# Performance work log

Hardware: AMD Instinct MI355X
Metric: run time of the kernel (lower is better)

Reference implementation:

```python
import jax, jax.numpy as jnp
import numpy as np

TEMP = 0.1
EPS = 1e-08

def _l2norm(x):
    # F.normalize semantics: x / max(||x||, 1e-12)
    n = jnp.linalg.norm(x, axis=-1, keepdims=True)
    return x / jnp.maximum(n, 1e-12)

def setup_inputs() -> dict:
    key = jax.random.key(0)
    k0, k1, k2, k3, k4 = jax.random.split(key, 5)
    B, Ph, Pw, D, O = 32, 32, 32, 512, 128
    P = Ph * Pw
    patch_features = jax.random.normal(k0, (B, Ph, Pw, D), jnp.float32)
    obj_features = jax.random.normal(k1, (B, O, D), jnp.float32)
    # e1i: each patch positively matched to one object (one-hot rows)
    idx = jax.random.randint(k2, (B, P), 0, O)
    e1i = jax.nn.one_hot(idx, O, dtype=jnp.float32)
    # e1j / e2j: sparse binary negative masks
    e1j = (jax.random.uniform(k3, (B, P, P)) < 0.1).astype(jnp.float32)
    e2j = (jax.random.uniform(k4, (B, P, O)) < 0.1).astype(jnp.float32)
    return {"patch_features": patch_features, "obj_features": obj_features,
            "e1i": e1i, "e1j": e1j, "e2j": e2j}

def reference(patch_features, obj_features, e1i, e1j, e2j):
    B, D = patch_features.shape[0], patch_features.shape[-1]
    pf = patch_features.reshape(B, -1, D)          # [B, P, D]
    pn = _l2norm(pf)
    on = _l2norm(obj_features)                     # [B, O, D]
    po_sim = jnp.einsum('bpd,bod->bpo', pn, on)    # patch-object cosine sim
    po_exp = jnp.exp(po_sim / TEMP)
    pp_exp = jnp.exp(jnp.einsum('bpd,bqd->bpq', pn, pn) / TEMP)
    delta_E1i_E2i = jnp.sum(e1i * po_exp, axis=-1)     # [B, P]
    sum_E1i_E1j = jnp.sum(e1j * pp_exp, axis=-1)
    sum_E1i_E2j = jnp.sum(e2j * po_exp, axis=-1)
    ratio = delta_E1i_E2i / (delta_E1i_E2i + sum_E1i_E1j + sum_E1i_E2j + EPS)
    loss_all = -jnp.log(ratio + EPS)                   # [B, P]
    valid = (jnp.sum(e1i, axis=-1) > 0).astype(loss_all.dtype)  # [B, P]
    n_valid = jnp.sum(valid)
    loss = jnp.sum(loss_all * valid) / n_valid
    matched = jnp.argmax(po_sim, axis=-1)              # [B, P]
    labels = jnp.take_along_axis(e1i, matched[..., None], axis=-1)[..., 0]
    matched_success_ratio = jnp.sum(labels * valid) / n_valid
    return loss, matched_success_ratio
```

## Files before the change

### kernel.cpp

```cpp
#include <hip/hip_runtime.h>
#include <hip/hip_bf16.h>

constexpr int BB = 32;
constexpr int P  = 1024;
constexpr int O  = 128;
constexpr int D  = 512;
constexpr float EPS = 1e-8f;
constexpr float SCL = 14.426950408889634f;

typedef __attribute__((ext_vector_type(8))) short short8;
typedef __attribute__((ext_vector_type(16))) float f32x16;

__device__ __forceinline__ unsigned short f2bf(float f) {
  __hip_bfloat16 h = __float2bfloat16(f);
  unsigned short u;
  __builtin_memcpy(&u, &h, sizeof(u));
  return u;
}

__device__ __forceinline__ void gld_lds16(const void* g, void* l) {
  __builtin_amdgcn_global_load_lds(
      (const __attribute__((address_space(1))) void*)g,
      (__attribute__((address_space(3))) void*)l, 16, 0, 0);
}

constexpr int FB = (BB * P + BB * O) / 4;
constexpr int JB = (BB * P) / 4;
__global__ __launch_bounds__(256) void prep2_kernel(
    const float* __restrict__ pf, const float* __restrict__ of,
    const float* __restrict__ e1i, const float* __restrict__ e1j,
    const float* __restrict__ e2j,
    __hip_bfloat16* __restrict__ pn, __hip_bfloat16* __restrict__ on,
    unsigned long long* __restrict__ bm1j, unsigned long long* __restrict__ bm2j,
    int* __restrict__ posr) {
  const int lane = threadIdx.x & 63;
  const int wid4 = threadIdx.x >> 6;
  const int bid  = blockIdx.x;

  if (bid < FB) {
    int row = bid * 4 + wid4;
    const float* src;
    __hip_bfloat16* dst;
    if (row < BB * P) {
      src = pf + (size_t)row * D;
      dst = pn + (size_t)row * D;
    } else {
      int r = row - BB * P;
      if (r >= BB * O) return;
      src = of + (size_t)r * D;
      dst = on + (size_t)r * D;
    }
    float4 v0 = *(const float4*)(src + lane * 8);
    float4 v1 = *(const float4*)(src + lane * 8 + 4);
    float ss = v0.x * v0.x + v0.y * v0.y + v0.z * v0.z + v0.w * v0.w +
               v1.x * v1.x + v1.y * v1.y + v1.z * v1.z + v1.w * v1.w;
    #pragma unroll
    for (int s = 1; s < 64; s <<= 1) ss += __shfl_xor(ss, s);
    float sc = 1.0f / fmaxf(sqrtf(ss), 1e-12f);
    short8 w;
    w[0] = (short)f2bf(v0.x * sc); w[1] = (short)f2bf(v0.y * sc);
    w[2] = (short)f2bf(v0.z * sc); w[3] = (short)f2bf(v0.w * sc);
    w[4] = (short)f2bf(v1.x * sc); w[5] = (short)f2bf(v1.y * sc);
    w[6] = (short)f2bf(v1.z * sc); w[7] = (short)f2bf(v1.w * sc);
    *reinterpret_cast<short8*>(dst + lane * 8) = w;
  } else if (bid < FB + JB) {
    const int row = (bid - FB) * 4 + wid4;
    const float* src = e1j + (size_t)row * P;
    #pragma unroll
    for (int it = 0; it < 16; ++it) {
      unsigned long long b = __ballot(src[it * 64 + lane] > 0.5f);
      if (lane == 0) bm1j[(size_t)row * 16 + it] = b;
    }
  } else {
    const int row = (bid - FB - JB) * 4 + wid4;
    unsigned long long b0 = __ballot(e1i[(size_t)row * O + lane] > 0.5f);
    unsigned long long b1 = __ballot(e1i[(size_t)row * O + 64 + lane] > 0.5f);
    unsigned long long d0 = __ballot(e2j[(size_t)row * O + lane] > 0.5f);
    unsigned long long d1 = __ballot(e2j[(size_t)row * O + 64 + lane] > 0.5f);
    if (lane == 0) {
      posr[row] = b0 ? (__ffsll(b0) - 1) : (b1 ? 63 + __ffsll(b1) : -1);
      bm2j[(size_t)row * 2]     = d0;
      bm2j[(size_t)row * 2 + 1] = d1;
    }
  }
}

__global__ __launch_bounds__(256, 3) void icl_main10(
    const __hip_bfloat16* __restrict__ pn, const __hip_bfloat16* __restrict__ on,
    const unsigned long long* __restrict__ bm1j,
    const unsigned long long* __restrict__ bm2j,
    const int* __restrict__ posr,
    float* __restrict__ d_row, float* __restrict__ s1_row,
    float* __restrict__ s2_row, unsigned long long* __restrict__ pk_row) {

  __shared__ __hip_bfloat16 As[128 * 64];
  __shared__ __hip_bfloat16 Bs[128 * 64];

  const int tid  = threadIdx.x;
  const int l    = tid & 63;
  const int wid  = tid >> 6;
  const int wr   = wid >> 1;
  const int wc   = wid & 1;
  const int half = l >> 5;
  const int l31  = l & 31;

  const int bid   = blockIdx.x;
  const int batch = bid & 31;
  const int unit  = bid >> 5;
  const int rt    = unit & 7;
  const int ct    = unit >> 3;
  const int row0  = rt * 128;

  const __hip_bfloat16* pnb = pn + (size_t)batch * P * D;
  const __hip_bfloat16* onb = on + (size_t)batch * O * D;
  const __hip_bfloat16* asrc = pnb + (size_t)row0 * D;
  const __hip_bfloat16* bsrc = (ct == 0) ? onb : pnb + (size_t)(ct - 1) * 128 * D;

  auto stage = [&](const __hip_bfloat16* __restrict__ src,
                   __hip_bfloat16* __restrict__ lds, int k0) {
    #pragma unroll
    for (int i = 0; i < 4; ++i) {
      int q = i * 256 + tid;
      int rr = q >> 3, c = q & 7;
      int gc = c ^ (rr & 7);
      gld_lds16(src + (size_t)rr * D + k0 + (gc << 3),
                (char*)lds + (size_t)(i * 256 + wid * 64) * 16);
    }
  };

  f32x16 acc[2][2];
  #pragma unroll
  for (int m = 0; m < 2; ++m)
    #pragma unroll
    for (int n = 0; n < 2; ++n)
      #pragma unroll
      for (int k = 0; k < 16; ++k) acc[m][n][k] = 0.f;

  for (int ks = 0; ks < 8; ++ks) {
    __syncthreads();
    stage(asrc, As, ks * 64);
    stage(bsrc, Bs, ks * 64);
    __syncthreads();
    #pragma unroll
    for (int kc = 0; kc < 4; ++kc) {
      const int ch = (kc << 1) | half;
      short8 af[2], bfr[2];
      #pragma unroll
      for (int m = 0; m < 2; ++m) {
        int row = wr * 64 + m * 32 + l31;
        af[m] = *reinterpret_cast<const short8*>(
            As + row * 64 + ((ch ^ (row & 7)) << 3));
      }
      #pragma unroll
      for (int n = 0; n < 2; ++n) {
        int col = wc * 64 + n * 32 + l31;
        bfr[n] = *reinterpret_cast<const short8*>(
            Bs + col * 64 + ((ch ^ (col & 7)) << 3));
      }
      #pragma unroll
      for (int m = 0; m < 2; ++m)
        #pragma unroll
        for (int n = 0; n < 2; ++n)
          acc[m][n] = __builtin_amdgcn_mfma_f32_32x32x16_bf16(
              af[m], bfr[n], acc[m][n], 0, 0, 0);
    }
  }

  if (ct == 0) {
    #pragma unroll
    for (int m = 0; m < 2; ++m) {
      #pragma unroll
      for (int r = 0; r < 16; ++r) {
        const int lrow = wr * 64 + m * 32 + (r & 3) + ((r >> 2) << 3) + (half << 2);
        const size_t grow = (size_t)batch * P + row0 + lrow;
        const int pos = posr[grow];
        const unsigned long long W2 = bm2j[grow * 2 + wc];
        const int c0 = wc * 64 + l31, c1 = c0 + 32;
        float s0 = acc[m][0][r], s1v = acc[m][1][r];
        float e0 = exp2f(s0 * SCL), e1v = exp2f(s1v * SCL);
        float dv  = (c0 == pos ? e0 : 0.f) + (c1 == pos ? e1v : 0.f);
        float s2v = (((W2 >> l31) & 1) ? e0 : 0.f) +
                    (((W2 >> (32 + l31)) & 1) ? e1v : 0.f);
        float mvv; int miv;
        if (s1v > s0) { mvv = s1v; miv = c1; } else { mvv = s0; miv = c0; }
        #pragma unroll
        for (int s = 1; s < 32; s <<= 1) {
          dv  += __shfl_xor(dv, s);
          s2v += __shfl_xor(s2v, s);
          float ov = __shfl_xor(mvv, s);
          int   oi = __shfl_xor(miv, s);
          if (ov > mvv || (ov == mvv && oi < miv)) { mvv = ov; miv = oi; }
        }
        if (l31 == 0) {
          if (dv != 0.f) atomicAdd(&d_row[grow], dv);
          atomicAdd(&s2_row[grow], s2v);
          unsigned long long pkv =
              ((unsigned long long)__float_as_uint(mvv + 2.0f) << 32) |
              (unsigned)(0xFFFFFFFFu - (unsigned)miv);
          atomicMax(&pk_row[grow], pkv);
        }
      }
    }
  } else {
    const int widx = (ct - 1) * 2 + wc;
    #pragma unroll
    for (int m = 0; m < 2; ++m) {
      #pragma unroll
      for (int r = 0; r < 16; ++r) {
        const int lrow = wr * 64 + m * 32 + (r & 3) + ((r >> 2) << 3) + (half << 2);
        const size_t grow = (size_t)batch * P + row0 + lrow;
        const unsigned long long W = bm1j[grow * 16 + widx];
        float v = (((W >> l31) & 1) ? exp2f(acc[m][0][r] * SCL) : 0.f) +
                  (((W >> (32 + l31)) & 1) ? exp2f(acc[m][1][r] * SCL) : 0.f);
        #pragma unroll
        for (int s = 1; s < 32; s <<= 1) v += __shfl_xor(v, s);
        if (l31 == 0 && v != 0.f) atomicAdd(&s1_row[grow], v);
      }
    }
  }
}

__global__ __launch_bounds__(256) void icl_reduce2(
    const float* __restrict__ d_row, const float* __restrict__ s1_row,
    const float* __restrict__ s2_row, const unsigned long long* __restrict__ pk_row,
    const int* __restrict__ posr, float* __restrict__ accum) {
  __shared__ float red[12];
  const int tid = threadIdx.x;
  const int row = blockIdx.x * 256 + tid;
  float d = d_row[row], a = s1_row[row], c = s2_row[row];
  int pos = posr[row];
  int miv = (int)(0xFFFFFFFFu - (unsigned)(pk_row[row] & 0xFFFFFFFFull));
  float valid = (pos >= 0) ? 1.f : 0.f;
  float ratio = d / (d + a + c + EPS);
  float lsum = -logf(ratio + EPS) * valid;
  float lbl  = (pos >= 0 && miv == pos) ? 1.f : 0.f;
  float vct  = valid;
  #pragma unroll
  for (int s = 1; s < 64; s <<= 1) {
    lsum += __shfl_xor(lsum, s);
    lbl  += __shfl_xor(lbl, s);
    vct  += __shfl_xor(vct, s);
  }
  const int wid = tid >> 6;
  if ((tid & 63) == 0) {
    red[wid * 3 + 0] = lsum;
    red[wid * 3 + 1] = lbl;
    red[wid * 3 + 2] = vct;
  }
  __syncthreads();
  if (tid == 0) {
    atomicAdd(&accum[0], red[0] + red[3] + red[6] + red[9]);
    atomicAdd(&accum[1], red[1] + red[4] + red[7] + red[10]);
    atomicAdd(&accum[2], red[2] + red[5] + red[8] + red[11]);
  }
}

__global__ void finalize_kernel(const float* __restrict__ accum,
                                float* __restrict__ out) {
  if (threadIdx.x == 0 && blockIdx.x == 0) {
    float nv = accum[2];
    out[0] = accum[0] / nv;
    out[1] = accum[1] / nv;
  }
}

__global__ __launch_bounds__(256) void norm_kernel(
    const float* __restrict__ pf, const float* __restrict__ of,
    float* __restrict__ invp, float* __restrict__ invo) {
  int lane = threadIdx.x & 63;
  int row = blockIdx.x * 4 + (threadIdx.x >> 6);
  const float* src;
  float* dst;
  if (row < BB * P) {
    src = pf + (size_t)row * D;
    dst = invp + row;
  } else {
    int r = row - BB * P;
    if (r >= BB * O) return;
    src = of + (size_t)r * D;
    dst = invo + r;
  }
  float ss = 0.f;
  #pragma unroll
  for (int i = 0; i < 2; ++i) {
    float4 v = *(const float4*)(src + (lane + 64 * i) * 4);
    ss += v.x * v.x + v.y * v.y + v.z * v.z + v.w * v.w;
  }
  #pragma unroll
  for (int s = 1; s < 64; s <<= 1) ss += __shfl_xor(ss, s);
  if (lane == 0) *dst = 1.0f / fmaxf(sqrtf(ss), 1e-12f);
}

__global__ __launch_bounds__(256) void icl_main_v1(
    const float* __restrict__ pf, const float* __restrict__ of,
    const float* __restrict__ e1i, const float* __restrict__ e1j,
    const float* __restrict__ e2j, const float* __restrict__ invp,
    const float* __restrict__ invo, float* __restrict__ accum) {
  constexpr int PT = 128, BK = 64;
  __shared__ __hip_bfloat16 As[PT * BK];
  __shared__ __hip_bfloat16 Bs[PT * BK];
  __shared__ float d_l[2][PT], s2_l[2][PT], ei_l[2][PT], s1_l[2][PT], mv_l[2][PT];
  __shared__ int   mi_l[2][PT];
  __shared__ float red[12];

  const int tid  = threadIdx.x;
  const int lane = tid & 63;
  const int wid  = tid >> 6;
  const int wr   = wid >> 1;
  const int wc   = wid & 1;
  const int half = lane >> 5;
  const int l31  = lane & 31;
  const int b    = blockIdx.x & 31;
  const int pt   = blockIdx.x >> 5;
  const int row0 = pt * PT;

  const float* pfb = pf + (size_t)b * P * D;
  const float* ofb = of + (size_t)b * O * D;
  const float* ivp = invp + b * P + row0;
  const float* ivq = invp + b * P;
  const float* ivo = invo + b * O;

  float s1p[2][16];
  #pragma unroll
  for (int m = 0; m < 2; ++m)
    #pragma unroll
    for (int r = 0; r < 16; ++r) s1p[m][r] = 0.f;

  auto stage = [&](const float* __restrict__ src, const float* __restrict__ inv,
                   __hip_bfloat16* __restrict__ lds, int k0) {
    #pragma unroll
    for (int i = 0; i < 8; ++i) {
      int c = i * 256 + tid;
      int rr = c >> 4, kc = c & 15;
      float4 v = *(const float4*)(src + (size_t)rr * D + k0 + (kc << 2));
      float s = inv[rr];
      int off = rr * BK + ((((kc >> 1) ^ (rr & 7)) << 3) | ((kc & 1) << 2));
      ushort4 w;
      w.x = f2bf(v.x * s);
      w.y = f2bf(v.y * s);
      w.z = f2bf(v.z * s);
      w.w = f2bf(v.w * s);
      *reinterpret_cast<ushort4*>(lds + off) = w;
    }
  };

  for (int ct = 0; ct < 9; ++ct) {
    const float* bsrc = (ct == 0) ? ofb : pfb + (size_t)(ct - 1) * 128 * D;
    const float* binv = (ct == 0) ? ivo : ivq + (ct - 1) * 128;

    f32x16 acc[2][2];
    #pragma unroll
    for (int m = 0; m < 2; ++m)
      #pragma unroll
      for (int n = 0; n < 2; ++n)
        #pragma unroll
        for (int k = 0; k < 16; ++k) acc[m][n][k] = 0.f;

    for (int ks = 0; ks < D / BK; ++ks) {
      __syncthreads();
      stage(pfb + (size_t)row0 * D, ivp, As, ks * BK);
      stage(bsrc, binv, Bs, ks * BK);
      __syncthreads();
      #pragma unroll
      for (int kc = 0; kc < 4; ++kc) {
        short8 af[2], bfr[2];
        #pragma unroll
        for (int m = 0; m < 2; ++m) {
          int row = wr * 64 + m * 32 + l31;
          af[m] = *reinterpret_cast<const short8*>(
              As + row * BK + ((((kc << 1) | half) ^ (row & 7)) << 3));
        }
        #pragma unroll
        for (int n = 0; n < 2; ++n) {
          int col = wc * 64 + n * 32 + l31;
          bfr[n] = *reinterpret_cast<const short8*>(
              Bs + col * BK + ((((kc << 1) | half) ^ (col & 7)) << 3));
        }
        #pragma unroll
        for (int m = 0; m < 2; ++m)
          #pragma unroll
          for (int n = 0; n < 2; ++n)
            acc[m][n] = __builtin_amdgcn_mfma_f32_32x32x16_bf16(
                af[m], bfr[n], acc[m][n], 0, 0, 0);
      }
    }

    if (ct == 0) {
      #pragma unroll
      for (int m = 0; m < 2; ++m) {
        #pragma unroll
        for (int r = 0; r < 16; ++r) {
          int lrow = wr * 64 + m * 32 + (r & 3) + ((r >> 2) << 3) + (half << 2);
          size_t base = ((size_t)b * P + row0 + lrow) * O;
          float dsum = 0.f, s2s = 0.f, eis = 0.f, mval = -1e30f;
          int midx = 0;
          #pragma unroll
          for (int n = 0; n < 2; ++n) {
            int col = wc * 64 + n * 32 + l31;
            float sim = acc[m][n][r];
            float e = exp2f(sim * SCL);
            float v1 = e1i[base + col];
            float v2 = e2j[base + col];
            dsum += v1 * e;
            s2s  += v2 * e;
            eis  += v1;
            if (sim > mval) { mval = sim; midx = col; }
          }
          #pragma unroll
          for (int s = 1; s < 32; s <<= 1) {
            dsum += __shfl_xor(dsum, s);
            s2s  += __shfl_xor(s2s, s);
            eis  += __shfl_xor(eis, s);
            float ov = __shfl_xor(mval, s);
            int   oi = __shfl_xor(midx, s);
            if (ov > mval || (ov == mval && oi < midx)) { mval = ov; midx = oi; }
          }
          if (l31 == 0) {
            d_l[wc][lrow] = dsum;
            s2_l[wc][lrow] = s2s;
            ei_l[wc][lrow] = eis;
            mv_l[wc][lrow] = mval;
            mi_l[wc][lrow] = midx;
          }
        }
      }
    } else {
      const int qbase = (ct - 1) * 128;
      #pragma unroll
      for (int m = 0; m < 2; ++m) {
        #pragma unroll
        for (int r = 0; r < 16; ++r) {
          int lrow = wr * 64 + m * 32 + (r & 3) + ((r >> 2) << 3) + (half << 2);
          size_t base = ((size_t)b * P + row0 + lrow) * P + qbase;
          float s = 0.f;
          #pragma unroll
          for (int n = 0; n < 2; ++n) {
            int col = wc * 64 + n * 32 + l31;
            s += e1j[base + col] * exp2f(acc[m][n][r] * SCL);
          }
          s1p[m][r] += s;
        }
      }
    }
  }

  #pragma unroll
  for (int m = 0; m < 2; ++m) {
    #pragma unroll
    for (int r = 0; r < 16; ++r) {
      float v = s1p[m][r];
      #pragma unroll
      for (int s = 1; s < 32; s <<= 1) v += __shfl_xor(v, s);
      if (l31 == 0) {
        int lrow = wr * 64 + m * 32 + (r & 3) + ((r >> 2) << 3) + (half << 2);
        s1_l[wc][lrow] = v;
      }
    }
  }
  __syncthreads();

  float lsum = 0.f, lbl = 0.f, vct = 0.f;
  if (tid < PT) {
    float delta = d_l[0][tid] + d_l[1][tid];
    float s2 = s2_l[0][tid] + s2_l[1][tid];
    float eis = ei_l[0][tid] + ei_l[1][tid];
    float s1 = s1_l[0][tid] + s1_l[1][tid];
    float m0 = mv_l[0][tid], m1 = mv_l[1][tid];
    int mi = (m1 > m0) ? mi_l[1][tid] : mi_l[0][tid];
    float valid = (eis > 0.f) ? 1.f : 0.f;
    float ratio = delta / (delta + s1 + s2 + EPS);
    float loss = -logf(ratio + EPS);
    float label = e1i[((size_t)b * P + row0 + tid) * O + mi];
    lsum = loss * valid;
    lbl  = label * valid;
    vct  = valid;
  }
  #pragma unroll
  for (int s = 1; s < 64; s <<= 1) {
    lsum += __shfl_xor(lsum, s);
    lbl  += __shfl_xor(lbl, s);
    vct  += __shfl_xor(vct, s);
  }
  if (lane == 0) {
    red[wid * 3 + 0] = lsum;
    red[wid * 3 + 1] = lbl;
    red[wid * 3 + 2] = vct;
  }
  __syncthreads();
  if (tid == 0) {
    float a = red[0] + red[3] + red[6] + red[9];
    float c = red[1] + red[4] + red[7] + red[10];
    float v = red[2] + red[5] + red[8] + red[11];
    atomicAdd(&accum[0], a);
    atomicAdd(&accum[1], c);
    atomicAdd(&accum[2], v);
  }
}

extern "C" void kernel_launch(void* const* d_in, const int* in_sizes, int n_in,
                              void* d_out, int out_size, void* d_ws, size_t ws_size,
                              hipStream_t stream) {
  const float* pf  = (const float*)d_in[0];
  const float* of  = (const float*)d_in[1];
  const float* e1i = (const float*)d_in[2];
  const float* e1j = (const float*)d_in[3];
  const float* e2j = (const float*)d_in[4];

  char* base = (char*)d_ws;
  constexpr size_t NR = (size_t)BB * P;
  float* accum               = (float*)base;
  float* d_row               = (float*)(base + 64);
  float* s1_row              = (float*)(base + 64 + 4 * NR);
  float* s2_row              = (float*)(base + 64 + 8 * NR);
  unsigned long long* pk_row = (unsigned long long*)(base + 64 + 12 * NR);
  unsigned long long* bm1j   = (unsigned long long*)(base + 64 + 20 * NR);
  unsigned long long* bm2j   = (unsigned long long*)(base + 64 + 148 * NR);
  int* posr                  = (int*)(base + 64 + 164 * NR);
  __hip_bfloat16* pn         = (__hip_bfloat16*)(base + 64 + 168 * NR);
  const size_t pn_bytes = (size_t)BB * P * D * 2;
  const size_t on_bytes = (size_t)BB * O * D * 2;
  __hip_bfloat16* on         = (__hip_bfloat16*)(base + 64 + 168 * NR + pn_bytes);
  const size_t need = 64 + 168 * NR + pn_bytes + on_bytes;

  if (ws_size >= need) {
    hipMemsetAsync(base, 0, 64 + 20 * NR, stream);
    prep2_kernel<<<FB + 2 * JB, 256, 0, stream>>>(pf, of, e1i, e1j, e2j,
                                                  pn, on, bm1j, bm2j, posr);
    icl_main10<<<BB * 72, 256, 0, stream>>>(pn, on, bm1j, bm2j, posr,
                                            d_row, s1_row, s2_row, pk_row);
    icl_reduce2<<<NR / 256, 256, 0, stream>>>(d_row, s1_row, s2_row, pk_row,
                                              posr, accum);
  } else {
    float* ws   = (float*)d_ws;
    float* invp = ws + 16;
    float* invo = ws + 16 + BB * P;
    hipMemsetAsync(accum, 0, 16 * sizeof(float), stream);
    norm_kernel<<<(BB * P + BB * O) / 4, 256, 0, stream>>>(pf, of, invp, invo);
    icl_main_v1<<<BB * (P / 128), 256, 0, stream>>>(pf, of, e1i, e1j, e2j,
                                                    invp, invo, accum);
  }
  finalize_kernel<<<1, 64, 0, stream>>>(accum, (float*)d_out);
}
```

Before: 176.6 us.

## Enlarge GEMM tiles to 256x256 with 512-thread blocks and vectorize e1j bitmask packing

The main kernel now uses 512-thread blocks. Patch-patch tiles grow from 128x128 to 256x256 with a 4x2 MFMA accumulator per wave, and patch-object tiles become 256x128. This raises arithmetic intensity and cuts redundant global/LDS traffic per output. The grid drops to 640 blocks. The prep kernel packs e1j masks using float4 loads and shuffles instead of per-element ballots. The larger tiles double LDS use and raise register pressure, and fewer blocks may reduce occupancy and load balance.

Measured after the change: 629.7 us. 257% more time.

```diff
diff --git a/kernel.cpp b/kernel.cpp
--- a/kernel.cpp
+++ b/kernel.cpp
@@ -66,11 +66,19 @@
   } else if (bid < FB + JB) {
     const int row = (bid - FB) * 4 + wid4;
     const float* src = e1j + (size_t)row * P;
-    #pragma unroll
-    for (int it = 0; it < 16; ++it) {
-      unsigned long long b = __ballot(src[it * 64 + lane] > 0.5f);
-      if (lane == 0) bm1j[(size_t)row * 16 + it] = b;
-    }
+    unsigned bits = 0;
+    #pragma unroll
+    for (int c = 0; c < 4; ++c) {
+      float4 v = *(const float4*)(src + lane * 16 + c * 4);
+      bits |= ((v.x > 0.5f) ? 1u : 0u) << (c * 4);
+      bits |= ((v.y > 0.5f) ? 1u : 0u) << (c * 4 + 1);
+      bits |= ((v.z > 0.5f) ? 1u : 0u) << (c * 4 + 2);
+      bits |= ((v.w > 0.5f) ? 1u : 0u) << (c * 4 + 3);
+    }
+    unsigned long long wbits = (unsigned long long)bits << ((lane & 3) * 16);
+    wbits |= __shfl_xor(wbits, 1);
+    wbits |= __shfl_xor(wbits, 2);
+    if ((lane & 3) == 0) bm1j[(size_t)row * 16 + (lane >> 2)] = wbits;
   } else {
     const int row = (bid - FB - JB) * 4 + wid4;
     unsigned long long b0 = __ballot(e1i[(size_t)row * O + lane] > 0.5f);
@@ -85,7 +93,7 @@
   }
 }
 
-__global__ __launch_bounds__(256, 3) void icl_main10(
+__global__ __launch_bounds__(512, 4) void icl_main12(
     const __hip_bfloat16* __restrict__ pn, const __hip_bfloat16* __restrict__ on,
     const unsigned long long* __restrict__ bm1j,
     const unsigned long long* __restrict__ bm2j,
@@ -93,80 +101,79 @@
     float* __restrict__ d_row, float* __restrict__ s1_row,
     float* __restrict__ s2_row, unsigned long long* __restrict__ pk_row) {
 
-  __shared__ __hip_bfloat16 As[128 * 64];
-  __shared__ __hip_bfloat16 Bs[128 * 64];
+  __shared__ __hip_bfloat16 As[256 * 64];
+  __shared__ __hip_bfloat16 Bs[256 * 64];
 
   const int tid  = threadIdx.x;
   const int l    = tid & 63;
   const int wid  = tid >> 6;
-  const int wr   = wid >> 1;
-  const int wc   = wid & 1;
   const int half = l >> 5;
   const int l31  = l & 31;
-
-  const int bid   = blockIdx.x;
-  const int batch = bid & 31;
-  const int unit  = bid >> 5;
-  const int rt    = unit & 7;
-  const int ct    = unit >> 3;
-  const int row0  = rt * 128;
-
-  const __hip_bfloat16* pnb = pn + (size_t)batch * P * D;
-  const __hip_bfloat16* onb = on + (size_t)batch * O * D;
-  const __hip_bfloat16* asrc = pnb + (size_t)row0 * D;
-  const __hip_bfloat16* bsrc = (ct == 0) ? onb : pnb + (size_t)(ct - 1) * 128 * D;
-
-  auto stage = [&](const __hip_bfloat16* __restrict__ src,
-                   __hip_bfloat16* __restrict__ lds, int k0) {
-    #pragma unroll
-    for (int i = 0; i < 4; ++i) {
-      int q = i * 256 + tid;
-      int rr = q >> 3, c = q & 7;
-      int gc = c ^ (rr & 7);
-      gld_lds16(src + (size_t)rr * D + k0 + (gc << 3),
-                (char*)lds + (size_t)(i * 256 + wid * 64) * 16);
-    }
-  };
-
-  f32x16 acc[2][2];
-  #pragma unroll
-  for (int m = 0; m < 2; ++m)
-    #pragma unroll
-    for (int n = 0; n < 2; ++n)
-      #pragma unroll
-      for (int k = 0; k < 16; ++k) acc[m][n][k] = 0.f;
-
-  for (int ks = 0; ks < 8; ++ks) {
-    __syncthreads();
-    stage(asrc, As, ks * 64);
-    stage(bsrc, Bs, ks * 64);
-    __syncthreads();
-    #pragma unroll
-    for (int kc = 0; kc < 4; ++kc) {
-      const int ch = (kc << 1) | half;
-      short8 af[2], bfr[2];
-      #pragma unroll
-      for (int m = 0; m < 2; ++m) {
-        int row = wr * 64 + m * 32 + l31;
-        af[m] = *reinterpret_cast<const short8*>(
-            As + row * 64 + ((ch ^ (row & 7)) << 3));
-      }
-      #pragma unroll
-      for (int n = 0; n < 2; ++n) {
-        int col = wc * 64 + n * 32 + l31;
-        bfr[n] = *reinterpret_cast<const short8*>(
-            Bs + col * 64 + ((ch ^ (col & 7)) << 3));
-      }
-      #pragma unroll
-      for (int m = 0; m < 2; ++m)
-        #pragma unroll
-        for (int n = 0; n < 2; ++n)
-          acc[m][n] = __builtin_amdgcn_mfma_f32_32x32x16_bf16(
-              af[m], bfr[n], acc[m][n], 0, 0, 0);
-    }
-  }
-
-  if (ct == 0) {
+  const int bid  = blockIdx.x;
+
+  if (bid < 128) {
+    const int batch = bid & 31;
+    const int rt    = bid >> 5;
+    const int row0  = rt * 256;
+    const int wr    = wid >> 1;
+    const int wc    = wid & 1;
+
+    const __hip_bfloat16* asrc = pn + (size_t)batch * P * D + (size_t)row0 * D;
+    const __hip_bfloat16* bsrc = on + (size_t)batch * O * D;
+
+    f32x16 acc[2][2];
+    #pragma unroll
+    for (int m = 0; m < 2; ++m)
+      #pragma unroll
+      for (int n = 0; n < 2; ++n)
+        #pragma unroll
+        for (int k = 0; k < 16; ++k) acc[m][n][k] = 0.f;
+
+    for (int ks = 0; ks < 8; ++ks) {
+      const int k0 = ks * 64;
+      __syncthreads();
+      #pragma unroll
+      for (int i = 0; i < 4; ++i) {
+        int q = i * 512 + tid;
+        int rr = q >> 3, c = q & 7;
+        int gc = c ^ (rr & 7);
+        gld_lds16(asrc + (size_t)rr * D + k0 + (gc << 3),
+                  (char*)As + (size_t)(i * 512 + wid * 64) * 16);
+      }
+      #pragma unroll
+      for (int i = 0; i < 2; ++i) {
+        int q = i * 512 + tid;
+        int rr = q >> 3, c = q & 7;
+        int gc = c ^ (rr & 7);
+        gld_lds16(bsrc + (size_t)rr * D + k0 + (gc << 3),
+                  (char*)Bs + (size_t)(i * 512 + wid * 64) * 16);
+      }
+      __syncthreads();
+      #pragma unroll
+      for (int kc = 0; kc < 4; ++kc) {
+        const int ch = (kc << 1) | half;
+        short8 af[2], bfr[2];
+        #pragma unroll
+        for (int m = 0; m < 2; ++m) {
+          int row = wr * 64 + m * 32 + l31;
+          af[m] = *reinterpret_cast<const short8*>(
+              As + row * 64 + ((ch ^ (row & 7)) << 3));
+        }
+        #pragma unroll
+        for (int n = 0; n < 2; ++n) {
+          int col = wc * 64 + n * 32 + l31;
+          bfr[n] = *reinterpret_cast<const short8*>(
+              Bs + col * 64 + ((ch ^ (col & 7)) << 3));
+        }
+        #pragma unroll
+        for (int m = 0; m < 2; ++m)
+          #pragma unroll
+          for (int n = 0; n < 2; ++n)
+            acc[m][n] = __builtin_amdgcn_mfma_f32_32x32x16_bf16(
+                af[m], bfr[n], acc[m][n], 0, 0, 0);
+      }
+    }
+
     #pragma unroll
     for (int m = 0; m < 2; ++m) {
       #pragma unroll
@@ -202,12 +209,77 @@
       }
     }
   } else {
-    const int widx = (ct - 1) * 2 + wc;
-    #pragma unroll
-    for (int m = 0; m < 2; ++m) {
+    const int pid   = bid - 128;
+    const int batch = pid & 31;
+    const int u     = pid >> 5;
+    const int rt    = u & 3;
+    const int ct    = u >> 2;
+    const int row0  = rt * 256;
+    const int pb    = ct * 256;
+    const int wr    = wid >> 2;
+    const int wcg   = wid & 3;
+
+    const __hip_bfloat16* pnb  = pn + (size_t)batch * P * D;
+    const __hip_bfloat16* asrc = pnb + (size_t)row0 * D;
+    const __hip_bfloat16* bsrc = pnb + (size_t)pb * D;
+
+    f32x16 acc[4][2];
+    #pragma unroll
+    for (int m = 0; m < 4; ++m)
+      #pragma unroll
+      for (int n = 0; n < 2; ++n)
+        #pragma unroll
+        for (int k = 0; k < 16; ++k) acc[m][n][k] = 0.f;
+
+    for (int ks = 0; ks < 8; ++ks) {
+      const int k0 = ks * 64;
+      __syncthreads();
+      #pragma unroll
+      for (int i = 0; i < 4; ++i) {
+        int q = i * 512 + tid;
+        int rr = q >> 3, c = q & 7;
+        int gc = c ^ (rr & 7);
+        gld_lds16(asrc + (size_t)rr * D + k0 + (gc << 3),
+                  (char*)As + (size_t)(i * 512 + wid * 64) * 16);
+      }
+      #pragma unroll
+      for (int i = 0; i < 4; ++i) {
+        int q = i * 512 + tid;
+        int rr = q >> 3, c = q & 7;
+        int gc = c ^ (rr & 7);
+        gld_lds16(bsrc + (size_t)rr * D + k0 + (gc << 3),
+                  (char*)Bs + (size_t)(i * 512 + wid * 64) * 16);
+      }
+      __syncthreads();
+      #pragma unroll
+      for (int kc = 0; kc < 4; ++kc) {
+        const int ch = (kc << 1) | half;
+        short8 bfr[2];
+        #pragma unroll
+        for (int n = 0; n < 2; ++n) {
+          int col = wcg * 64 + n * 32 + l31;
+          bfr[n] = *reinterpret_cast<const short8*>(
+              Bs + col * 64 + ((ch ^ (col & 7)) << 3));
+        }
+        #pragma unroll
+        for (int m = 0; m < 4; ++m) {
+          int row = wr * 128 + m * 32 + l31;
+          short8 af = *reinterpret_cast<const short8*>(
+              As + row * 64 + ((ch ^ (row & 7)) << 3));
+          #pragma unroll
+          for (int n = 0; n < 2; ++n)
+            acc[m][n] = __builtin_amdgcn_mfma_f32_32x32x16_bf16(
+                af, bfr[n], acc[m][n], 0, 0, 0);
+        }
+      }
+    }
+
+    const int widx = ct * 4 + wcg;
+    #pragma unroll
+    for (int m = 0; m < 4; ++m) {
       #pragma unroll
       for (int r = 0; r < 16; ++r) {
-        const int lrow = wr * 64 + m * 32 + (r & 3) + ((r >> 2) << 3) + (half << 2);
+        const int lrow = wr * 128 + m * 32 + (r & 3) + ((r >> 2) << 3) + (half << 2);
         const size_t grow = (size_t)batch * P + row0 + lrow;
         const unsigned long long W = bm1j[grow * 16 + widx];
         float v = (((W >> l31) & 1) ? exp2f(acc[m][0][r] * SCL) : 0.f) +
@@ -526,8 +598,8 @@
     hipMemsetAsync(base, 0, 64 + 20 * NR, stream);
     prep2_kernel<<<FB + 2 * JB, 256, 0, stream>>>(pf, of, e1i, e1j, e2j,
                                                   pn, on, bm1j, bm2j, posr);
-    icl_main10<<<BB * 72, 256, 0, stream>>>(pn, on, bm1j, bm2j, posr,
-                                            d_row, s1_row, s2_row, pk_row);
+    icl_main12<<<640, 512, 0, stream>>>(pn, on, bm1j, bm2j, posr,
+                                        d_row, s1_row, s2_row, pk_row);
     icl_reduce2<<<NR / 256, 256, 0, stream>>>(d_row, s1_row, s2_row, pk_row,
                                               posr, accum);
   } else {
```
